# Kernel optimization log

Hardware: AMD Instinct MI355X
Metric: run time of the kernel (lower is better)

The kernel has to match this reference:

```python
import jax, jax.numpy as jnp
import numpy as np

H = 2048        # hidden_size
I = 5632        # intermediate_size (SwiGLU)
E = 8           # num_experts
K = 2           # top_k
B, S = 4, 2048


def setup_inputs() -> dict:
    key = jax.random.key(0)
    ks = jax.random.split(key, 6)
    s_h = 1.0 / np.sqrt(H)
    s_i = 1.0 / np.sqrt(I)
    return {
        "hidden_states": jax.random.normal(ks[0], (B, S, H), dtype=jnp.float32),
        "Wr": jax.random.normal(ks[1], (H, E), dtype=jnp.float32) * s_h,   # router linear weight
        "br": jnp.zeros((E,), dtype=jnp.float32),                           # router bias
        "Wg": jax.random.normal(ks[2], (E, H, I), dtype=jnp.float32) * s_h, # gate_proj per expert
        "Wu": jax.random.normal(ks[3], (E, H, I), dtype=jnp.float32) * s_h, # up_proj per expert
        "Wd": jax.random.normal(ks[4], (E, I, H), dtype=jnp.float32) * s_i, # down_proj per expert
    }


def reference(hidden_states, Wr, br, Wg, Wu, Wd):
    b, s, h = hidden_states.shape
    xf = hidden_states.reshape(b * s, h)                      # [T, H]

    # Router (eval mode: no noise, no dropout)
    router_logits = xf @ Wr + br                              # [T, E]
    probs = jax.nn.softmax(router_logits, axis=-1)
    w, idx = jax.lax.top_k(probs, K)                          # [T, K]
    w = w / jnp.sum(w, axis=-1, keepdims=True)                # renormalize top-k weights

    out = jnp.zeros_like(xf)
    for e in range(E):
        # per-token combine weight for expert e (sums duplicate k-slots, as the torch loop does)
        we = jnp.sum(w * (idx == e), axis=-1)                 # [T]
        # SwiGLU expert: down(silu(gate(x)) * up(x))
        expert_out = (jax.nn.silu(xf @ Wg[e]) * (xf @ Wu[e])) @ Wd[e]  # [T, H]
        out = out + expert_out * we[:, None]
    output = out.reshape(b, s, h)
    return output, router_logits
```

## Files before the change

kernel.cpp:

```cpp
#include <hip/hip_runtime.h>

#define Hdim 2048
#define Idim 5632
#define NEXP 8
#define NTOK 8192
#define NROW 16384
#define RCAP 18432
#define MT256 72

#define MI_NTILES   0
#define MI_TOTAL    1
#define MI_COUNT    2
#define MI_CURSOR   10
#define MI_OFF      18
#define MI_TILEEXP  32
#define MI_ROWTOK   128
#define MI_ROWW     18560
#define MI_TOPKID   36992
#define MI_TOPKW    53376
#define META_ZERO_BYTES (36992u * 4u)

#define XG_OFF   (1ull << 19)
#define WGT_OFF  (73ull  << 20)
#define WUT_OFF  (249ull << 20)
#define HB_OFF   (425ull << 20)
#define WDT_OFF  WGT_OFF

typedef __attribute__((ext_vector_type(8))) short s8v;
typedef __attribute__((ext_vector_type(4))) float f4v;

#define BAR()  asm volatile("s_barrier" ::: "memory")
#define VMW2() asm volatile("s_waitcnt vmcnt(2)" ::: "memory")

__device__ __forceinline__ unsigned short f2bf(float f) {
  unsigned int u = __float_as_uint(f);
  u += 0x7fffu + ((u >> 16) & 1u);
  return (unsigned short)(u >> 16);
}
__device__ __forceinline__ unsigned int pack2(float lo, float hi) {
  return (__float_as_uint(lo) >> 16) | (__float_as_uint(hi) & 0xffff0000u);
}
__device__ __forceinline__ void glds16(const short* gp, short* lp) {
  __builtin_amdgcn_global_load_lds(
      (const __attribute__((address_space(1))) void*)gp,
      (__attribute__((address_space(3))) void*)lp, 16, 0, 0);
}

__global__ __launch_bounds__(256) void router_kernel(
    const float* __restrict__ x, const float* __restrict__ Wr,
    const float* __restrict__ br, float* __restrict__ logits,
    int* __restrict__ meta)
{
  int wv = threadIdx.x >> 6, lane = threadIdx.x & 63;
  int t = blockIdx.x * 4 + wv;
  const float* xr = x + (size_t)t * Hdim;
  float acc[8];
#pragma unroll
  for (int e = 0; e < 8; ++e) acc[e] = 0.f;
  for (int i = lane; i < Hdim; i += 64) {
    float xv = xr[i];
    const float4 w0 = *(const float4*)(Wr + (size_t)i * 8);
    const float4 w1 = *(const float4*)(Wr + (size_t)i * 8 + 4);
    acc[0] += xv * w0.x; acc[1] += xv * w0.y; acc[2] += xv * w0.z; acc[3] += xv * w0.w;
    acc[4] += xv * w1.x; acc[5] += xv * w1.y; acc[6] += xv * w1.z; acc[7] += xv * w1.w;
  }
#pragma unroll
  for (int off = 32; off > 0; off >>= 1)
#pragma unroll
    for (int e = 0; e < 8; ++e) acc[e] += __shfl_down(acc[e], off);
  if (lane == 0) {
    float l[8];
#pragma unroll
    for (int e = 0; e < 8; ++e) { l[e] = acc[e] + br[e]; logits[(size_t)t * 8 + e] = l[e]; }
    int i1 = 0;
#pragma unroll
    for (int e = 1; e < 8; ++e) if (l[e] > l[i1]) i1 = e;
    int i2 = -1;
#pragma unroll
    for (int e = 0; e < 8; ++e) if (e != i1 && (i2 < 0 || l[e] > l[i2])) i2 = e;
    float p2 = __expf(l[i2] - l[i1]);
    float s = 1.f + p2;
    meta[MI_TOPKID + t * 2]     = i1;
    meta[MI_TOPKID + t * 2 + 1] = i2;
    float* tw = (float*)(meta + MI_TOPKW);
    tw[t * 2] = 1.f / s; tw[t * 2 + 1] = p2 / s;
    atomicAdd(&meta[MI_COUNT + i1], 1);
    atomicAdd(&meta[MI_COUNT + i2], 1);
  }
}

__global__ void offsets_kernel(int* __restrict__ meta)
{
  __shared__ int soff[9];
  if (threadIdx.x == 0) {
    int off = 0;
#pragma unroll
    for (int e = 0; e < 8; ++e) {
      soff[e] = off;
      meta[MI_OFF + e] = off;
      meta[MI_CURSOR + e] = off;
      int c = meta[MI_COUNT + e];
      off += (c + 255) & ~255;
    }
    soff[8] = off;
    meta[MI_OFF + 8] = off;
    meta[MI_TOTAL] = off;
    meta[MI_NTILES] = off >> 8;
  }
  __syncthreads();
  int tile = threadIdx.x;
  if (tile < MT256) {
    int r = tile << 8;
    int e = 7;
    for (int q = 7; q >= 0; --q) if (r < soff[q + 1]) e = q;
    meta[MI_TILEEXP + tile] = e;
  }
}

__global__ __launch_bounds__(256) void scatter_kernel(int* __restrict__ meta)
{
  int idx = blockIdx.x * 256 + threadIdx.x;
  int e = meta[MI_TOPKID + idx];
  float w = ((const float*)(meta + MI_TOPKW))[idx];
  int pos = atomicAdd(&meta[MI_CURSOR + e], 1);
  meta[MI_ROWTOK + pos] = idx >> 1;
  ((float*)(meta + MI_ROWW))[pos] = w;
}

__global__ __launch_bounds__(256) void gather_kernel(
    const float* __restrict__ x, short* __restrict__ Xg,
    const int* __restrict__ meta)
{
  int r = blockIdx.x;
  int tok = meta[MI_ROWTOK + r];
  int i = threadIdx.x * 8;
  const float* src = x + (size_t)tok * Hdim + i;
  float4 a = *(const float4*)src;
  float4 b = *(const float4*)(src + 4);
  union { s8v v; unsigned short us[8]; } o;
  o.us[0] = f2bf(a.x); o.us[1] = f2bf(a.y); o.us[2] = f2bf(a.z); o.us[3] = f2bf(a.w);
  o.us[4] = f2bf(b.x); o.us[5] = f2bf(b.y); o.us[6] = f2bf(b.z); o.us[7] = f2bf(b.w);
  *(s8v*)(Xg + (size_t)r * Hdim + i) = o.v;
}

__global__ __launch_bounds__(256) void convT_kernel(
    const float* __restrict__ W, short* __restrict__ T, int K, int N)
{
  __shared__ float lds[64][65];
  int ntn = N >> 6, ntk = K >> 6;
  int per_e = ntn * ntk;
  int e = blockIdx.x / per_e;
  int r = blockIdx.x % per_e;
  int tn = r % ntn, tk = r / ntn;
  const float* We = W + (size_t)e * K * N;
  short* Te = T + (size_t)e * K * N;
  int n0 = tn << 6, k0 = tk << 6;
  int tid = threadIdx.x;
  int c = tid & 63, rr = tid >> 6;
#pragma unroll
  for (int i = 0; i < 16; ++i) {
    int k = i * 4 + rr;
    lds[c][k] = We[(size_t)(k0 + k) * N + n0 + c];
  }
  __syncthreads();
  int kp = tid & 31, nb = tid >> 5;
#pragma unroll
  for (int i = 0; i < 8; ++i) {
    int n = i * 8 + nb;
    float2 f = *(const float2*)&lds[n][kp * 2];
    unsigned int u = pack2(f.x, f.y);
    *(unsigned int*)((char*)Te + ((size_t)(n0 + n) * K + k0) * 2 + kp * 4) = u;
  }
}


#define ISSUE_A2(buf, h, kt) do { size_t kk_ = (size_t)(kt) * 64;                          \
  glds16(pA + (size_t)((h) * 128      ) * strideA + kk_, &sA[(buf)][(h) * 8192 + ldst]);   \
  glds16(pA + (size_t)((h) * 128 + 64 ) * strideA + kk_, &sA[(buf)][(h) * 8192 + 4096 + ldst]); } while (0)
#define ISSUE_B2(arr, pB, buf, kt) do { size_t kk_ = (size_t)(kt) * 64;                    \
  glds16((pB) + kk_,                          &arr[(buf)][ldst]);                          \
  glds16((pB) + (size_t)64 * strideA + kk_,   &arr[(buf)][4096 + ldst]); } while (0)

__global__ __launch_bounds__(512, 2) void gateup_kernel(
    const short* __restrict__ Xg, const short* __restrict__ WgT,
    const short* __restrict__ WuT, short* __restrict__ Hbuf,
    const int* __restrict__ meta)
{
  const int NT = Idim / 128;
  int wg = (blockIdx.x & 7) * (MT256 / 8 * NT) + (blockIdx.x >> 3);
  int chunk = wg / (8 * NT);
  int rem   = wg % (8 * NT);
  int mtile = chunk * 8 + (rem & 7);
  int ntile = rem >> 3;
  if (mtile >= meta[MI_NTILES]) return;
  int e = meta[MI_TILEEXP + mtile];
  int n0 = ntile * 128;
  const size_t strideA = Hdim;

  __shared__ short sA[2][16384];
  __shared__ short sG[2][8192];
  __shared__ short sU[2][8192];

  int tid = threadIdx.x;
  int lane = tid & 63, wv = tid >> 6;
  int wm = wv >> 1, wn = wv & 1;
  int lr = lane & 15, lg = lane >> 4;
  int ldst = wv * 512;

  int srow = tid >> 3;
  int kc = ((tid & 7) ^ (srow & 7)) * 8;
  const short* pA = Xg  + (size_t)(mtile * 256) * Hdim + (size_t)srow * Hdim + kc;
  const short* pG = WgT + (size_t)e * Idim * Hdim + (size_t)(n0 + srow) * Hdim + kc;
  const short* pU = WuT + (size_t)e * Idim * Hdim + (size_t)(n0 + srow) * Hdim + kc;

  int aoff[4][2], boff[4][2];
#pragma unroll
  for (int mi = 0; mi < 4; ++mi) {
    int R = wm * 64 + mi * 16 + lr;
#pragma unroll
    for (int ks = 0; ks < 2; ++ks) aoff[mi][ks] = R * 64 + (((ks * 4 + lg) ^ (R & 7)) << 3);
  }
#pragma unroll
  for (int ni = 0; ni < 4; ++ni) {
    int R = wn * 64 + ni * 16 + lr;
#pragma unroll
    for (int ks = 0; ks < 2; ++ks) boff[ni][ks] = R * 64 + (((ks * 4 + lg) ^ (R & 7)) << 3);
  }

  f4v AG[4][4], AU[4][4];
  f4v z = {0.f, 0.f, 0.f, 0.f};
#pragma unroll
  for (int a1 = 0; a1 < 4; ++a1)
#pragma unroll
    for (int b1 = 0; b1 < 4; ++b1) { AG[a1][b1] = z; AU[a1][b1] = z; }

  const int NKT = Hdim / 64;

  ISSUE_A2(0, 0, 0); ISSUE_A2(0, 1, 0);
  ISSUE_B2(sG, pG, 0, 0); ISSUE_B2(sU, pU, 0, 0);
  ISSUE_A2(1, 0, 1);
  VMW2(); BAR();

#define GU_HALF(CUR, T)                                                                    \
  do {                                                                                     \
    int nx1 = (T) + 1; if (nx1 >= NKT) nx1 -= NKT;                                         \
    int nx2 = (T) + 2; if (nx2 >= NKT) nx2 -= NKT;                                         \
    s8v a_[4][2], g0_[2][2], g1_[2][2], u0_[2][2], u1_[2][2];                              \
                                                 \
    _Pragma("unroll") for (int mi = 0; mi < 4; ++mi)                                       \
      _Pragma("unroll") for (int ks = 0; ks < 2; ++ks)                                     \
        a_[mi][ks] = *(const s8v*)&sA[CUR][aoff[mi][ks]];                                  \
    _Pragma("unroll") for (int ni = 0; ni < 2; ++ni)                                       \
      _Pragma("unroll") for (int ks = 0; ks < 2; ++ks)                                     \
        g0_[ni][ks] = *(const s8v*)&sG[CUR][boff[ni][ks]];                                 \
    ISSUE_A2((CUR) ^ 1, 1, nx1);                                                           \
    BAR(); __builtin_amdgcn_s_setprio(1);                                                  \
    _Pragma("unroll") for (int mi = 0; mi < 4; ++mi)                                       \
      _Pragma("unroll") for (int ni = 0; ni < 2; ++ni)                                     \
        _Pragma("unroll") for (int ks = 0; ks < 2; ++ks)                                   \
          AG[mi][ni] = __builtin_amdgcn_mfma_f32_16x16x32_bf16(a_[mi][ks], g0_[ni][ks],    \
                                                               AG[mi][ni], 0, 0, 0);       \
    __builtin_amdgcn_s_setprio(0); BAR();                                                  \
                                             \
    _Pragma("unroll") for (int ni = 0; ni < 2; ++ni)                                       \
      _Pragma("unroll") for (int ks = 0; ks < 2; ++ks) {                                   \
        g1_[ni][ks] = *(const s8v*)&sG[CUR][boff[2 + ni][ks]];                             \
        u0_[ni][ks] = *(const s8v*)&sU[CUR][boff[ni][ks]];                                 \
      }                                                                                    \
    ISSUE_B2(sG, pG, (CUR) ^ 1, nx1);                                                      \
    BAR(); __builtin_amdgcn_s_setprio(1);                                                  \
    _Pragma("unroll") for (int mi = 0; mi < 4; ++mi)                                       \
      _Pragma("unroll") for (int ni = 0; ni < 2; ++ni)                                     \
        _Pragma("unroll") for (int ks = 0; ks < 2; ++ks)                                   \
          AG[mi][2 + ni] = __builtin_amdgcn_mfma_f32_16x16x32_bf16(a_[mi][ks], g1_[ni][ks],\
                                                                   AG[mi][2 + ni], 0, 0, 0);\
    __builtin_amdgcn_s_setprio(0); BAR();                                                  \
                                           \
    _Pragma("unroll") for (int ni = 0; ni < 2; ++ni)                                       \
      _Pragma("unroll") for (int ks = 0; ks < 2; ++ks)                                     \
        u1_[ni][ks] = *(const s8v*)&sU[CUR][boff[2 + ni][ks]];                             \
    ISSUE_B2(sU, pU, (CUR) ^ 1, nx1);                                                      \
    BAR(); __builtin_amdgcn_s_setprio(1);                                                  \
    _Pragma("unroll") for (int mi = 0; mi < 4; ++mi)                                       \
      _Pragma("unroll") for (int ni = 0; ni < 2; ++ni)                                     \
        _Pragma("unroll") for (int ks = 0; ks < 2; ++ks)                                   \
          AU[mi][ni] = __builtin_amdgcn_mfma_f32_16x16x32_bf16(a_[mi][ks], u0_[ni][ks],    \
                                                               AU[mi][ni], 0, 0, 0);       \
    __builtin_amdgcn_s_setprio(0); BAR();                                                  \
                                         \
    ISSUE_A2(CUR, 0, nx2);                                                                 \
    VMW2();                                                                                \
    BAR(); __builtin_amdgcn_s_setprio(1);                                                  \
    _Pragma("unroll") for (int mi = 0; mi < 4; ++mi)                                       \
      _Pragma("unroll") for (int ni = 0; ni < 2; ++ni)                                     \
        _Pragma("unroll") for (int ks = 0; ks < 2; ++ks)                                   \
          AU[mi][2 + ni] = __builtin_amdgcn_mfma_f32_16x16x32_bf16(a_[mi][ks], u1_[ni][ks],\
                                                                   AU[mi][2 + ni], 0, 0, 0);\
    __builtin_amdgcn_s_setprio(0); BAR();                                                  \
  } while (0)

  for (int t = 0; t < NKT; t += 2) {
    GU_HALF(0, t);
    GU_HALF(1, t + 1);
  }
#undef GU_HALF

  int row0 = mtile * 256 + wm * 64;
  int col0 = n0 + wn * 64;
#pragma unroll
  for (int mi = 0; mi < 4; ++mi) {
#pragma unroll
    for (int ni = 0; ni < 4; ++ni) {
      int col = col0 + ni * 16 + lr;
#pragma unroll
      for (int r = 0; r < 4; ++r) {
        int row = row0 + mi * 16 + lg * 4 + r;
        float g = AG[mi][ni][r], u = AU[mi][ni][r];
        float h = g / (1.f + __expf(-g)) * u;
        Hbuf[(size_t)row * Idim + col] = (short)f2bf(h);
      }
    }
  }
}

__global__ __launch_bounds__(512, 2) void down_kernel(
    const short* __restrict__ Hbuf, const short* __restrict__ WdT,
    float* __restrict__ out, const int* __restrict__ meta)
{
  const int NT = Hdim / 128;
  int wg = (blockIdx.x & 7) * (MT256 / 8 * NT) + (blockIdx.x >> 3);
  int chunk = wg / (8 * NT);
  int rem   = wg % (8 * NT);
  int mtile = chunk * 8 + (rem & 7);
  int ntile = rem >> 3;
  if (mtile >= meta[MI_NTILES]) return;
  int e = meta[MI_TILEEXP + mtile];
  int n0 = ntile * 128;
  const size_t strideA = Idim;

  __shared__ short sA[2][16384];
  __shared__ short sB[2][8192];

  int tid = threadIdx.x;
  int lane = tid & 63, wv = tid >> 6;
  int wm = wv >> 1, wn = wv & 1;
  int lr = lane & 15, lg = lane >> 4;
  int ldst = wv * 512;

  int srow = tid >> 3;
  int kc = ((tid & 7) ^ (srow & 7)) * 8;
  const short* pA = Hbuf + (size_t)(mtile * 256) * Idim + (size_t)srow * Idim + kc;
  const short* pB = WdT  + (size_t)e * Hdim * Idim + (size_t)(n0 + srow) * Idim + kc;

  int aoff[4][2], boff[4][2];
#pragma unroll
  for (int mi = 0; mi < 4; ++mi) {
    int R = wm * 64 + mi * 16 + lr;
#pragma unroll
    for (int ks = 0; ks < 2; ++ks) aoff[mi][ks] = R * 64 + (((ks * 4 + lg) ^ (R & 7)) << 3);
  }
#pragma unroll
  for (int ni = 0; ni < 4; ++ni) {
    int R = wn * 64 + ni * 16 + lr;
#pragma unroll
    for (int ks = 0; ks < 2; ++ks) boff[ni][ks] = R * 64 + (((ks * 4 + lg) ^ (R & 7)) << 3);
  }

  f4v AC[4][4];
  f4v z = {0.f, 0.f, 0.f, 0.f};
#pragma unroll
  for (int a1 = 0; a1 < 4; ++a1)
#pragma unroll
    for (int b1 = 0; b1 < 4; ++b1) AC[a1][b1] = z;

  const int NKT = Idim / 64;

  ISSUE_A2(0, 0, 0); ISSUE_A2(0, 1, 0);
  ISSUE_B2(sB, pB, 0, 0);
  ISSUE_A2(1, 0, 1);
  VMW2(); BAR();

#define DN_PHASE(CUR, NI, EXTRA)                                                           \
  do {                                                                                     \
    EXTRA;                                                                                 \
    BAR(); __builtin_amdgcn_s_setprio(1);                                                  \
    _Pragma("unroll") for (int mi = 0; mi < 4; ++mi)                                       \
      _Pragma("unroll") for (int ks = 0; ks < 2; ++ks)                                     \
        AC[mi][NI] = __builtin_amdgcn_mfma_f32_16x16x32_bf16(a_[mi][ks], b_[NI][ks],       \
                                                             AC[mi][NI], 0, 0, 0);         \
    __builtin_amdgcn_s_setprio(0); BAR();                                                  \
  } while (0)

#define DN_HALF(CUR, T)                                                                    \
  do {                                                                                     \
    int nx1 = (T) + 1; if (nx1 >= NKT) nx1 -= NKT;                                         \
    int nx2 = (T) + 2; if (nx2 >= NKT) nx2 -= NKT;                                         \
    s8v a_[4][2], b_[4][2];                                                                \
                                                                \
    _Pragma("unroll") for (int mi = 0; mi < 4; ++mi)                                       \
      _Pragma("unroll") for (int ks = 0; ks < 2; ++ks)                                     \
        a_[mi][ks] = *(const s8v*)&sA[CUR][aoff[mi][ks]];                                  \
    _Pragma("unroll") for (int ni = 0; ni < 2; ++ni)                                       \
      _Pragma("unroll") for (int ks = 0; ks < 2; ++ks)                                     \
        b_[ni][ks] = *(const s8v*)&sB[CUR][boff[ni][ks]];                                  \
    DN_PHASE(CUR, 0, ISSUE_A2((CUR) ^ 1, 1, nx1));                                         \
                                                                    \
    DN_PHASE(CUR, 1, {                                                                     \
      _Pragma("unroll") for (int ni = 2; ni < 4; ++ni)                                     \
        _Pragma("unroll") for (int ks = 0; ks < 2; ++ks)                                   \
          b_[ni][ks] = *(const s8v*)&sB[CUR][boff[ni][ks]];                                \
      ISSUE_B2(sB, pB, (CUR) ^ 1, nx1); });                                                \
    DN_PHASE(CUR, 2, {});                                                                  \
    DN_PHASE(CUR, 3, { ISSUE_A2(CUR, 0, nx2); VMW2(); });                                  \
  } while (0)

  for (int t = 0; t < NKT; t += 2) {
    DN_HALF(0, t);
    DN_HALF(1, t + 1);
  }
#undef DN_HALF
#undef DN_PHASE

  int row0 = mtile * 256 + wm * 64;
  int col0 = n0 + wn * 64;
  const int* rowtok = meta + MI_ROWTOK;
  const float* roww = (const float*)(meta + MI_ROWW);
#pragma unroll
  for (int mi = 0; mi < 4; ++mi) {
#pragma unroll
    for (int r = 0; r < 4; ++r) {
      int row = row0 + mi * 16 + lg * 4 + r;
      int tok = rowtok[row];
      float w = roww[row];
      float* orow = out + (size_t)tok * Hdim + col0 + lr;
#pragma unroll
      for (int ni = 0; ni < 4; ++ni)
        atomicAdd(orow + ni * 16, w * AC[mi][ni][r]);
    }
  }
}

extern "C" void kernel_launch(void* const* d_in, const int* in_sizes, int n_in,
                              void* d_out, int out_size, void* d_ws, size_t ws_size,
                              hipStream_t stream)
{
  (void)in_sizes; (void)n_in; (void)out_size; (void)ws_size;
  const float* x  = (const float*)d_in[0];
  const float* Wr = (const float*)d_in[1];
  const float* br = (const float*)d_in[2];
  const float* Wg = (const float*)d_in[3];
  const float* Wu = (const float*)d_in[4];
  const float* Wd = (const float*)d_in[5];
  float* out = (float*)d_out;
  float* logits = out + (size_t)NTOK * Hdim;
  int* meta = (int*)d_ws;
  short* Xg   = (short*)((char*)d_ws + XG_OFF);
  short* WgT  = (short*)((char*)d_ws + WGT_OFF);
  short* WuT  = (short*)((char*)d_ws + WUT_OFF);
  short* WdT  = (short*)((char*)d_ws + WDT_OFF);
  short* Hbuf = (short*)((char*)d_ws + HB_OFF);

  hipMemsetAsync(d_out, 0, (size_t)NTOK * Hdim * sizeof(float), stream);
  hipMemsetAsync(d_ws, 0, META_ZERO_BYTES, stream);

  const int convBlocks = NEXP * (Idim / 64) * (Hdim / 64);

  router_kernel <<<NTOK / 4, 256, 0, stream>>>(x, Wr, br, logits, meta);
  offsets_kernel<<<1, 256, 0, stream>>>(meta);
  scatter_kernel<<<NROW / 256, 256, 0, stream>>>(meta);
  gather_kernel <<<RCAP, 256, 0, stream>>>(x, Xg, meta);
  convT_kernel  <<<convBlocks, 256, 0, stream>>>(Wg, WgT, Hdim, Idim);
  convT_kernel  <<<convBlocks, 256, 0, stream>>>(Wu, WuT, Hdim, Idim);
  gateup_kernel <<<MT256 * (Idim / 128), 512, 0, stream>>>(Xg, WgT, WuT, Hbuf, meta);
  convT_kernel  <<<convBlocks, 256, 0, stream>>>(Wd, WdT, Idim, Hdim);
  down_kernel   <<<MT256 * (Hdim / 128), 512, 0, stream>>>(Hbuf, WdT, out, meta);
}
```

Before: 2.298 ms.

## Widen down-proj tile to 256 columns and batch per-stage global-to-LDS loads

The down-projection kernel now computes a 256x256 output tile per workgroup instead of 256x128. This halves how often the A (hidden) operand is re-read and halves the number of atomic-add tiles per row. Both GEMM kernels replace their interleaved half-stage prefetches with one full-stage load burst per k-tile, waited on with vmcnt(8) and an lgkmcnt(0) fence. The cost is more accumulator registers (AC grows to 4x8), double the sB LDS footprint, and fewer workgroups in the down kernel, which may lower occupancy.

```diff
diff --git a/kernel.cpp b/kernel.cpp
--- a/kernel.cpp
+++ b/kernel.cpp
@@ -29,8 +29,11 @@
 typedef __attribute__((ext_vector_type(8))) short s8v;
 typedef __attribute__((ext_vector_type(4))) float f4v;
 
-#define BAR()  asm volatile("s_barrier" ::: "memory")
-#define VMW2() asm volatile("s_waitcnt vmcnt(2)" ::: "memory")
+#define BAR()   asm volatile("s_barrier" ::: "memory")
+#define VMW8()  asm volatile("s_waitcnt vmcnt(8)" ::: "memory")
+#define LGKM0() asm volatile("s_waitcnt lgkmcnt(0)" ::: "memory")
+#define PRIO1() __builtin_amdgcn_s_setprio(1)
+#define PRIO0() __builtin_amdgcn_s_setprio(0)
 
 __device__ __forceinline__ unsigned short f2bf(float f) {
   unsigned int u = __float_as_uint(f);
@@ -174,12 +177,8 @@
 }
 
 
-#define ISSUE_A2(buf, h, kt) do { size_t kk_ = (size_t)(kt) * 64;                          \
-  glds16(pA + (size_t)((h) * 128      ) * strideA + kk_, &sA[(buf)][(h) * 8192 + ldst]);   \
-  glds16(pA + (size_t)((h) * 128 + 64 ) * strideA + kk_, &sA[(buf)][(h) * 8192 + 4096 + ldst]); } while (0)
-#define ISSUE_B2(arr, pB, buf, kt) do { size_t kk_ = (size_t)(kt) * 64;                    \
-  glds16((pB) + kk_,                          &arr[(buf)][ldst]);                          \
-  glds16((pB) + (size_t)64 * strideA + kk_,   &arr[(buf)][4096 + ldst]); } while (0)
+#define STG(arr, pX, buf, r, kk) \
+  glds16((pX) + (size_t)(r) * 64 * strideA + (kk), &arr[(buf)][(r) * 4096 + ldst])
 
 __global__ __launch_bounds__(512, 2) void gateup_kernel(
     const short* __restrict__ Xg, const short* __restrict__ WgT,
@@ -236,74 +235,75 @@
 
   const int NKT = Hdim / 64;
 
-  ISSUE_A2(0, 0, 0); ISSUE_A2(0, 1, 0);
-  ISSUE_B2(sG, pG, 0, 0); ISSUE_B2(sU, pU, 0, 0);
-  ISSUE_A2(1, 0, 1);
-  VMW2(); BAR();
-
-#define GU_HALF(CUR, T)                                                                    \
+#define GU_STAGE(buf, kt) do { size_t kk_ = (size_t)(kt) * 64;  \
+    STG(sA, pA, buf, 0, kk_); STG(sA, pA, buf, 1, kk_);         \
+    STG(sA, pA, buf, 2, kk_); STG(sA, pA, buf, 3, kk_);         \
+    STG(sG, pG, buf, 0, kk_); STG(sG, pG, buf, 1, kk_);         \
+    STG(sU, pU, buf, 0, kk_); STG(sU, pU, buf, 1, kk_); } while (0)
+
+  GU_STAGE(0, 0); GU_STAGE(1, 1);
+  VMW8(); BAR();
+
+#define GU_TILE(CUR, T)                                                                    \
   do {                                                                                     \
-    int nx1 = (T) + 1; if (nx1 >= NKT) nx1 -= NKT;                                         \
     int nx2 = (T) + 2; if (nx2 >= NKT) nx2 -= NKT;                                         \
     s8v a_[4][2], g0_[2][2], g1_[2][2], u0_[2][2], u1_[2][2];                              \
-                                                 \
+                                                                      \
     _Pragma("unroll") for (int mi = 0; mi < 4; ++mi)                                       \
       _Pragma("unroll") for (int ks = 0; ks < 2; ++ks)                                     \
         a_[mi][ks] = *(const s8v*)&sA[CUR][aoff[mi][ks]];                                  \
     _Pragma("unroll") for (int ni = 0; ni < 2; ++ni)                                       \
       _Pragma("unroll") for (int ks = 0; ks < 2; ++ks)                                     \
         g0_[ni][ks] = *(const s8v*)&sG[CUR][boff[ni][ks]];                                 \
-    ISSUE_A2((CUR) ^ 1, 1, nx1);                                                           \
-    BAR(); __builtin_amdgcn_s_setprio(1);                                                  \
+    BAR(); PRIO1();                                                                        \
     _Pragma("unroll") for (int mi = 0; mi < 4; ++mi)                                       \
       _Pragma("unroll") for (int ni = 0; ni < 2; ++ni)                                     \
         _Pragma("unroll") for (int ks = 0; ks < 2; ++ks)                                   \
           AG[mi][ni] = __builtin_amdgcn_mfma_f32_16x16x32_bf16(a_[mi][ks], g0_[ni][ks],    \
                                                                AG[mi][ni], 0, 0, 0);       \
-    __builtin_amdgcn_s_setprio(0); BAR();                                                  \
-                                             \
+    PRIO0(); BAR();                                                                        \
+                                                                     \
     _Pragma("unroll") for (int ni = 0; ni < 2; ++ni)                                       \
       _Pragma("unroll") for (int ks = 0; ks < 2; ++ks) {                                   \
         g1_[ni][ks] = *(const s8v*)&sG[CUR][boff[2 + ni][ks]];                             \
         u0_[ni][ks] = *(const s8v*)&sU[CUR][boff[ni][ks]];                                 \
       }                                                                                    \
-    ISSUE_B2(sG, pG, (CUR) ^ 1, nx1);                                                      \
-    BAR(); __builtin_amdgcn_s_setprio(1);                                                  \
+    BAR(); PRIO1();                                                                        \
     _Pragma("unroll") for (int mi = 0; mi < 4; ++mi)                                       \
       _Pragma("unroll") for (int ni = 0; ni < 2; ++ni)                                     \
         _Pragma("unroll") for (int ks = 0; ks < 2; ++ks)                                   \
           AG[mi][2 + ni] = __builtin_amdgcn_mfma_f32_16x16x32_bf16(a_[mi][ks], g1_[ni][ks],\
                                                                    AG[mi][2 + ni], 0, 0, 0);\
-    __builtin_amdgcn_s_setprio(0); BAR();                                                  \
-                                           \
+    PRIO0(); BAR();                                                                        \
+          \
     _Pragma("unroll") for (int ni = 0; ni < 2; ++ni)                                       \
       _Pragma("unroll") for (int ks = 0; ks < 2; ++ks)                                     \
         u1_[ni][ks] = *(const s8v*)&sU[CUR][boff[2 + ni][ks]];                             \
-    ISSUE_B2(sU, pU, (CUR) ^ 1, nx1);                                                      \
-    BAR(); __builtin_amdgcn_s_setprio(1);                                                  \
+    BAR(); PRIO1();                                                                        \
     _Pragma("unroll") for (int mi = 0; mi < 4; ++mi)                                       \
       _Pragma("unroll") for (int ni = 0; ni < 2; ++ni)                                     \
         _Pragma("unroll") for (int ks = 0; ks < 2; ++ks)                                   \
           AU[mi][ni] = __builtin_amdgcn_mfma_f32_16x16x32_bf16(a_[mi][ks], u0_[ni][ks],    \
                                                                AU[mi][ni], 0, 0, 0);       \
-    __builtin_amdgcn_s_setprio(0); BAR();                                                  \
-                                         \
-    ISSUE_A2(CUR, 0, nx2);                                                                 \
-    VMW2();                                                                                \
-    BAR(); __builtin_amdgcn_s_setprio(1);                                                  \
+    PRIO0(); LGKM0(); BAR();                                                               \
+         \
+    GU_STAGE(CUR, nx2);                                                                    \
+    VMW8();                                                                                \
+    BAR(); PRIO1();                                                                        \
     _Pragma("unroll") for (int mi = 0; mi < 4; ++mi)                                       \
       _Pragma("unroll") for (int ni = 0; ni < 2; ++ni)                                     \
         _Pragma("unroll") for (int ks = 0; ks < 2; ++ks)                                   \
           AU[mi][2 + ni] = __builtin_amdgcn_mfma_f32_16x16x32_bf16(a_[mi][ks], u1_[ni][ks],\
                                                                    AU[mi][2 + ni], 0, 0, 0);\
-    __builtin_amdgcn_s_setprio(0); BAR();                                                  \
+    PRIO0(); BAR();                                                                        \
   } while (0)
 
   for (int t = 0; t < NKT; t += 2) {
-    GU_HALF(0, t);
-    GU_HALF(1, t + 1);
-  }
-#undef GU_HALF
+    GU_TILE(0, t);
+    GU_TILE(1, t + 1);
+  }
+#undef GU_TILE
+#undef GU_STAGE
 
   int row0 = mtile * 256 + wm * 64;
   int col0 = n0 + wn * 64;
@@ -327,7 +327,7 @@
     const short* __restrict__ Hbuf, const short* __restrict__ WdT,
     float* __restrict__ out, const int* __restrict__ meta)
 {
-  const int NT = Hdim / 128;
+  const int NT = Hdim / 256;
   int wg = (blockIdx.x & 7) * (MT256 / 8 * NT) + (blockIdx.x >> 3);
   int chunk = wg / (8 * NT);
   int rem   = wg % (8 * NT);
@@ -335,11 +335,11 @@
   int ntile = rem >> 3;
   if (mtile >= meta[MI_NTILES]) return;
   int e = meta[MI_TILEEXP + mtile];
-  int n0 = ntile * 128;
+  int n0 = ntile * 256;
   const size_t strideA = Idim;
 
   __shared__ short sA[2][16384];
-  __shared__ short sB[2][8192];
+  __shared__ short sB[2][16384];
 
   int tid = threadIdx.x;
   int lane = tid & 63, wv = tid >> 6;
@@ -352,7 +352,7 @@
   const short* pA = Hbuf + (size_t)(mtile * 256) * Idim + (size_t)srow * Idim + kc;
   const short* pB = WdT  + (size_t)e * Hdim * Idim + (size_t)(n0 + srow) * Idim + kc;
 
-  int aoff[4][2], boff[4][2];
+  int aoff[4][2], boff[8][2];
 #pragma unroll
   for (int mi = 0; mi < 4; ++mi) {
     int R = wm * 64 + mi * 16 + lr;
@@ -360,69 +360,77 @@
     for (int ks = 0; ks < 2; ++ks) aoff[mi][ks] = R * 64 + (((ks * 4 + lg) ^ (R & 7)) << 3);
   }
 #pragma unroll
-  for (int ni = 0; ni < 4; ++ni) {
-    int R = wn * 64 + ni * 16 + lr;
+  for (int ni = 0; ni < 8; ++ni) {
+    int R = wn * 128 + ni * 16 + lr;
 #pragma unroll
     for (int ks = 0; ks < 2; ++ks) boff[ni][ks] = R * 64 + (((ks * 4 + lg) ^ (R & 7)) << 3);
   }
 
-  f4v AC[4][4];
+  f4v AC[4][8];
   f4v z = {0.f, 0.f, 0.f, 0.f};
 #pragma unroll
   for (int a1 = 0; a1 < 4; ++a1)
 #pragma unroll
-    for (int b1 = 0; b1 < 4; ++b1) AC[a1][b1] = z;
+    for (int b1 = 0; b1 < 8; ++b1) AC[a1][b1] = z;
 
   const int NKT = Idim / 64;
 
-  ISSUE_A2(0, 0, 0); ISSUE_A2(0, 1, 0);
-  ISSUE_B2(sB, pB, 0, 0);
-  ISSUE_A2(1, 0, 1);
-  VMW2(); BAR();
-
-#define DN_PHASE(CUR, NI, EXTRA)                                                           \
+#define DN_STAGE(buf, kt) do { size_t kk_ = (size_t)(kt) * 64;  \
+    STG(sA, pA, buf, 0, kk_); STG(sA, pA, buf, 1, kk_);         \
+    STG(sA, pA, buf, 2, kk_); STG(sA, pA, buf, 3, kk_);         \
+    STG(sB, pB, buf, 0, kk_); STG(sB, pB, buf, 1, kk_);         \
+    STG(sB, pB, buf, 2, kk_); STG(sB, pB, buf, 3, kk_); } while (0)
+
+  DN_STAGE(0, 0); DN_STAGE(1, 1);
+  VMW8(); BAR();
+
+#define DN_MFMA(NI0)                                                                       \
+    BAR(); PRIO1();                                                                        \
+    _Pragma("unroll") for (int mi = 0; mi < 4; ++mi)                                       \
+      _Pragma("unroll") for (int nj = 0; nj < 2; ++nj)                                     \
+        _Pragma("unroll") for (int ks = 0; ks < 2; ++ks)                                   \
+          AC[mi][(NI0) + nj] = __builtin_amdgcn_mfma_f32_16x16x32_bf16(                    \
+              a_[mi][ks], b_[(NI0) + nj][ks], AC[mi][(NI0) + nj], 0, 0, 0);                \
+    PRIO0()
+
+#define DN_TILE(CUR, T)                                                                    \
   do {                                                                                     \
-    EXTRA;                                                                                 \
-    BAR(); __builtin_amdgcn_s_setprio(1);                                                  \
-    _Pragma("unroll") for (int mi = 0; mi < 4; ++mi)                                       \
-      _Pragma("unroll") for (int ks = 0; ks < 2; ++ks)                                     \
-        AC[mi][NI] = __builtin_amdgcn_mfma_f32_16x16x32_bf16(a_[mi][ks], b_[NI][ks],       \
-                                                             AC[mi][NI], 0, 0, 0);         \
-    __builtin_amdgcn_s_setprio(0); BAR();                                                  \
-  } while (0)
-
-#define DN_HALF(CUR, T)                                                                    \
-  do {                                                                                     \
-    int nx1 = (T) + 1; if (nx1 >= NKT) nx1 -= NKT;                                         \
     int nx2 = (T) + 2; if (nx2 >= NKT) nx2 -= NKT;                                         \
-    s8v a_[4][2], b_[4][2];                                                                \
-                                                                \
+    s8v a_[4][2], b_[8][2];                                                                \
+                                                                     \
     _Pragma("unroll") for (int mi = 0; mi < 4; ++mi)                                       \
       _Pragma("unroll") for (int ks = 0; ks < 2; ++ks)                                     \
         a_[mi][ks] = *(const s8v*)&sA[CUR][aoff[mi][ks]];                                  \
     _Pragma("unroll") for (int ni = 0; ni < 2; ++ni)                                       \
       _Pragma("unroll") for (int ks = 0; ks < 2; ++ks)                                     \
         b_[ni][ks] = *(const s8v*)&sB[CUR][boff[ni][ks]];                                  \
-    DN_PHASE(CUR, 0, ISSUE_A2((CUR) ^ 1, 1, nx1));                                         \
-                                                                    \
-    DN_PHASE(CUR, 1, {                                                                     \
-      _Pragma("unroll") for (int ni = 2; ni < 4; ++ni)                                     \
-        _Pragma("unroll") for (int ks = 0; ks < 2; ++ks)                                   \
-          b_[ni][ks] = *(const s8v*)&sB[CUR][boff[ni][ks]];                                \
-      ISSUE_B2(sB, pB, (CUR) ^ 1, nx1); });                                                \
-    DN_PHASE(CUR, 2, {});                                                                  \
-    DN_PHASE(CUR, 3, { ISSUE_A2(CUR, 0, nx2); VMW2(); });                                  \
+    DN_MFMA(0); BAR();                                                                     \
+                                                                         \
+    _Pragma("unroll") for (int ni = 2; ni < 4; ++ni)                                       \
+      _Pragma("unroll") for (int ks = 0; ks < 2; ++ks)                                     \
+        b_[ni][ks] = *(const s8v*)&sB[CUR][boff[ni][ks]];                                  \
+    DN_MFMA(2); BAR();                                                                     \
+                                       \
+    _Pragma("unroll") for (int ni = 4; ni < 8; ++ni)                                       \
+      _Pragma("unroll") for (int ks = 0; ks < 2; ++ks)                                     \
+        b_[ni][ks] = *(const s8v*)&sB[CUR][boff[ni][ks]];                                  \
+    DN_MFMA(4); LGKM0(); BAR();                                                            \
+                                                          \
+    DN_STAGE(CUR, nx2);                                                                    \
+    VMW8();                                                                                \
+    DN_MFMA(6); BAR();                                                                     \
   } while (0)
 
   for (int t = 0; t < NKT; t += 2) {
-    DN_HALF(0, t);
-    DN_HALF(1, t + 1);
-  }
-#undef DN_HALF
-#undef DN_PHASE
+    DN_TILE(0, t);
+    DN_TILE(1, t + 1);
+  }
+#undef DN_TILE
+#undef DN_MFMA
+#undef DN_STAGE
 
   int row0 = mtile * 256 + wm * 64;
-  int col0 = n0 + wn * 64;
+  int col0 = n0 + wn * 128;
   const int* rowtok = meta + MI_ROWTOK;
   const float* roww = (const float*)(meta + MI_ROWW);
 #pragma unroll
@@ -434,7 +442,7 @@
       float w = roww[row];
       float* orow = out + (size_t)tok * Hdim + col0 + lr;
 #pragma unroll
-      for (int ni = 0; ni < 4; ++ni)
+      for (int ni = 0; ni < 8; ++ni)
         atomicAdd(orow + ni * 16, w * AC[mi][ni][r]);
     }
   }
@@ -473,5 +481,5 @@
   convT_kernel  <<<convBlocks, 256, 0, stream>>>(Wu, WuT, Hdim, Idim);
   gateup_kernel <<<MT256 * (Idim / 128), 512, 0, stream>>>(Xg, WgT, WuT, Hbuf, meta);
   convT_kernel  <<<convBlocks, 256, 0, stream>>>(Wd, WdT, Idim, Hdim);
-  down_kernel   <<<MT256 * (Hdim / 128), 512, 0, stream>>>(Hbuf, WdT, out, meta);
-}
+  down_kernel   <<<MT256 * (Hdim / 256), 512, 0, stream>>>(Hbuf, WdT, out, meta);
+}
```

Result: no change. 2.256 ms (-1.8%).

## Load A operand directly from global into registers, stage only weights in LDS

Applied to the files above, without the earlier changes.

Both the gate/up and down GEMM kernels stop staging the activation (A) tile through shared memory. Each wave now reads its A fragments straight from global memory into registers, and only the weight tiles are double-buffered in LDS through a simpler one-stage-ahead pipeline that waits with vmcnt(0). The block-to-tile swizzle also changes from groups of 8 M-tiles to groups of 4. The aim is to free LDS and cut barrier and LDS traffic. The cost is that the global A loads are exposed to latency with little overlap, since each stage waits for all loads, and A is re-read by both N-halves of the waves.

```diff
diff --git a/kernel.cpp b/kernel.cpp
--- a/kernel.cpp
+++ b/kernel.cpp
@@ -29,8 +29,10 @@
 typedef __attribute__((ext_vector_type(8))) short s8v;
 typedef __attribute__((ext_vector_type(4))) float f4v;
 
-#define BAR()  asm volatile("s_barrier" ::: "memory")
-#define VMW2() asm volatile("s_waitcnt vmcnt(2)" ::: "memory")
+#define BAR()   asm volatile("s_barrier" ::: "memory")
+#define VMW0()  asm volatile("s_waitcnt vmcnt(0)" ::: "memory")
+#define PRIO1() __builtin_amdgcn_s_setprio(1)
+#define PRIO0() __builtin_amdgcn_s_setprio(0)
 
 __device__ __forceinline__ unsigned short f2bf(float f) {
   unsigned int u = __float_as_uint(f);
@@ -174,30 +176,21 @@
 }
 
 
-#define ISSUE_A2(buf, h, kt) do { size_t kk_ = (size_t)(kt) * 64;                          \
-  glds16(pA + (size_t)((h) * 128      ) * strideA + kk_, &sA[(buf)][(h) * 8192 + ldst]);   \
-  glds16(pA + (size_t)((h) * 128 + 64 ) * strideA + kk_, &sA[(buf)][(h) * 8192 + 4096 + ldst]); } while (0)
-#define ISSUE_B2(arr, pB, buf, kt) do { size_t kk_ = (size_t)(kt) * 64;                    \
-  glds16((pB) + kk_,                          &arr[(buf)][ldst]);                          \
-  glds16((pB) + (size_t)64 * strideA + kk_,   &arr[(buf)][4096 + ldst]); } while (0)
-
 __global__ __launch_bounds__(512, 2) void gateup_kernel(
     const short* __restrict__ Xg, const short* __restrict__ WgT,
     const short* __restrict__ WuT, short* __restrict__ Hbuf,
     const int* __restrict__ meta)
 {
   const int NT = Idim / 128;
-  int wg = (blockIdx.x & 7) * (MT256 / 8 * NT) + (blockIdx.x >> 3);
-  int chunk = wg / (8 * NT);
-  int rem   = wg % (8 * NT);
-  int mtile = chunk * 8 + (rem & 7);
-  int ntile = rem >> 3;
+  int wg = (blockIdx.x & 7) * ((MT256 * NT) / 8) + (blockIdx.x >> 3);
+  int chunk = wg / (4 * NT);
+  int rem   = wg % (4 * NT);
+  int mtile = chunk * 4 + (rem & 3);
+  int ntile = rem >> 2;
   if (mtile >= meta[MI_NTILES]) return;
   int e = meta[MI_TILEEXP + mtile];
   int n0 = ntile * 128;
-  const size_t strideA = Hdim;
-
-  __shared__ short sA[2][16384];
+
   __shared__ short sG[2][8192];
   __shared__ short sU[2][8192];
 
@@ -209,17 +202,15 @@
 
   int srow = tid >> 3;
   int kc = ((tid & 7) ^ (srow & 7)) * 8;
-  const short* pA = Xg  + (size_t)(mtile * 256) * Hdim + (size_t)srow * Hdim + kc;
   const short* pG = WgT + (size_t)e * Idim * Hdim + (size_t)(n0 + srow) * Hdim + kc;
   const short* pU = WuT + (size_t)e * Idim * Hdim + (size_t)(n0 + srow) * Hdim + kc;
 
-  int aoff[4][2], boff[4][2];
-#pragma unroll
-  for (int mi = 0; mi < 4; ++mi) {
-    int R = wm * 64 + mi * 16 + lr;
-#pragma unroll
-    for (int ks = 0; ks < 2; ++ks) aoff[mi][ks] = R * 64 + (((ks * 4 + lg) ^ (R & 7)) << 3);
-  }
+  const short* pAm[4];
+#pragma unroll
+  for (int mi = 0; mi < 4; ++mi)
+    pAm[mi] = Xg + (size_t)(mtile * 256 + wm * 64 + mi * 16 + lr) * Hdim + lg * 8;
+
+  int boff[4][2];
 #pragma unroll
   for (int ni = 0; ni < 4; ++ni) {
     int R = wn * 64 + ni * 16 + lr;
@@ -236,74 +227,63 @@
 
   const int NKT = Hdim / 64;
 
-  ISSUE_A2(0, 0, 0); ISSUE_A2(0, 1, 0);
-  ISSUE_B2(sG, pG, 0, 0); ISSUE_B2(sU, pU, 0, 0);
-  ISSUE_A2(1, 0, 1);
-  VMW2(); BAR();
-
-#define GU_HALF(CUR, T)                                                                    \
-  do {                                                                                     \
-    int nx1 = (T) + 1; if (nx1 >= NKT) nx1 -= NKT;                                         \
-    int nx2 = (T) + 2; if (nx2 >= NKT) nx2 -= NKT;                                         \
-    s8v a_[4][2], g0_[2][2], g1_[2][2], u0_[2][2], u1_[2][2];                              \
-                                                 \
-    _Pragma("unroll") for (int mi = 0; mi < 4; ++mi)                                       \
-      _Pragma("unroll") for (int ks = 0; ks < 2; ++ks)                                     \
-        a_[mi][ks] = *(const s8v*)&sA[CUR][aoff[mi][ks]];                                  \
-    _Pragma("unroll") for (int ni = 0; ni < 2; ++ni)                                       \
-      _Pragma("unroll") for (int ks = 0; ks < 2; ++ks)                                     \
-        g0_[ni][ks] = *(const s8v*)&sG[CUR][boff[ni][ks]];                                 \
-    ISSUE_A2((CUR) ^ 1, 1, nx1);                                                           \
-    BAR(); __builtin_amdgcn_s_setprio(1);                                                  \
-    _Pragma("unroll") for (int mi = 0; mi < 4; ++mi)                                       \
-      _Pragma("unroll") for (int ni = 0; ni < 2; ++ni)                                     \
-        _Pragma("unroll") for (int ks = 0; ks < 2; ++ks)                                   \
-          AG[mi][ni] = __builtin_amdgcn_mfma_f32_16x16x32_bf16(a_[mi][ks], g0_[ni][ks],    \
-                                                               AG[mi][ni], 0, 0, 0);       \
-    __builtin_amdgcn_s_setprio(0); BAR();                                                  \
-                                             \
-    _Pragma("unroll") for (int ni = 0; ni < 2; ++ni)                                       \
-      _Pragma("unroll") for (int ks = 0; ks < 2; ++ks) {                                   \
-        g1_[ni][ks] = *(const s8v*)&sG[CUR][boff[2 + ni][ks]];                             \
-        u0_[ni][ks] = *(const s8v*)&sU[CUR][boff[ni][ks]];                                 \
-      }                                                                                    \
-    ISSUE_B2(sG, pG, (CUR) ^ 1, nx1);                                                      \
-    BAR(); __builtin_amdgcn_s_setprio(1);                                                  \
-    _Pragma("unroll") for (int mi = 0; mi < 4; ++mi)                                       \
-      _Pragma("unroll") for (int ni = 0; ni < 2; ++ni)                                     \
-        _Pragma("unroll") for (int ks = 0; ks < 2; ++ks)                                   \
-          AG[mi][2 + ni] = __builtin_amdgcn_mfma_f32_16x16x32_bf16(a_[mi][ks], g1_[ni][ks],\
-                                                                   AG[mi][2 + ni], 0, 0, 0);\
-    __builtin_amdgcn_s_setprio(0); BAR();                                                  \
-                                           \
-    _Pragma("unroll") for (int ni = 0; ni < 2; ++ni)                                       \
-      _Pragma("unroll") for (int ks = 0; ks < 2; ++ks)                                     \
-        u1_[ni][ks] = *(const s8v*)&sU[CUR][boff[2 + ni][ks]];                             \
-    ISSUE_B2(sU, pU, (CUR) ^ 1, nx1);                                                      \
-    BAR(); __builtin_amdgcn_s_setprio(1);                                                  \
-    _Pragma("unroll") for (int mi = 0; mi < 4; ++mi)                                       \
-      _Pragma("unroll") for (int ni = 0; ni < 2; ++ni)                                     \
-        _Pragma("unroll") for (int ks = 0; ks < 2; ++ks)                                   \
-          AU[mi][ni] = __builtin_amdgcn_mfma_f32_16x16x32_bf16(a_[mi][ks], u0_[ni][ks],    \
-                                                               AU[mi][ni], 0, 0, 0);       \
-    __builtin_amdgcn_s_setprio(0); BAR();                                                  \
-                                         \
-    ISSUE_A2(CUR, 0, nx2);                                                                 \
-    VMW2();                                                                                \
-    BAR(); __builtin_amdgcn_s_setprio(1);                                                  \
-    _Pragma("unroll") for (int mi = 0; mi < 4; ++mi)                                       \
-      _Pragma("unroll") for (int ni = 0; ni < 2; ++ni)                                     \
-        _Pragma("unroll") for (int ks = 0; ks < 2; ++ks)                                   \
-          AU[mi][2 + ni] = __builtin_amdgcn_mfma_f32_16x16x32_bf16(a_[mi][ks], u1_[ni][ks],\
-                                                                   AU[mi][2 + ni], 0, 0, 0);\
-    __builtin_amdgcn_s_setprio(0); BAR();                                                  \
-  } while (0)
-
-  for (int t = 0; t < NKT; t += 2) {
-    GU_HALF(0, t);
-    GU_HALF(1, t + 1);
-  }
-#undef GU_HALF
+#define GU_STAGE(buf, kt) do { size_t kk_ = (size_t)(kt) * 64;                     \
+    glds16(pG + kk_,                     &sG[buf][ldst]);                          \
+    glds16(pG + (size_t)64 * Hdim + kk_, &sG[buf][4096 + ldst]);                   \
+    glds16(pU + kk_,                     &sU[buf][ldst]);                          \
+    glds16(pU + (size_t)64 * Hdim + kk_, &sU[buf][4096 + ldst]); } while (0)
+
+  GU_STAGE(0, 0);
+
+#pragma unroll 2
+  for (int t = 0; t < NKT; ++t) {
+    int cur = t & 1;
+    int nx = (t + 1 < NKT) ? (t + 1) : 0;
+    int k0 = t * 64;
+    VMW0();
+    BAR();
+    s8v a_[4][2];
+#pragma unroll
+    for (int mi = 0; mi < 4; ++mi)
+#pragma unroll
+      for (int ks = 0; ks < 2; ++ks)
+        a_[mi][ks] = *(const s8v*)(pAm[mi] + k0 + ks * 32);
+    __builtin_amdgcn_sched_barrier(0);
+    GU_STAGE(cur ^ 1, nx);
+    s8v g_[4][2];
+#pragma unroll
+    for (int ni = 0; ni < 4; ++ni)
+#pragma unroll
+      for (int ks = 0; ks < 2; ++ks)
+        g_[ni][ks] = *(const s8v*)&sG[cur][boff[ni][ks]];
+    PRIO1();
+#pragma unroll
+    for (int mi = 0; mi < 4; ++mi)
+#pragma unroll
+      for (int ni = 0; ni < 4; ++ni)
+#pragma unroll
+        for (int ks = 0; ks < 2; ++ks)
+          AG[mi][ni] = __builtin_amdgcn_mfma_f32_16x16x32_bf16(a_[mi][ks], g_[ni][ks],
+                                                               AG[mi][ni], 0, 0, 0);
+    PRIO0();
+    s8v u_[4][2];
+#pragma unroll
+    for (int ni = 0; ni < 4; ++ni)
+#pragma unroll
+      for (int ks = 0; ks < 2; ++ks)
+        u_[ni][ks] = *(const s8v*)&sU[cur][boff[ni][ks]];
+    PRIO1();
+#pragma unroll
+    for (int mi = 0; mi < 4; ++mi)
+#pragma unroll
+      for (int ni = 0; ni < 4; ++ni)
+#pragma unroll
+        for (int ks = 0; ks < 2; ++ks)
+          AU[mi][ni] = __builtin_amdgcn_mfma_f32_16x16x32_bf16(a_[mi][ks], u_[ni][ks],
+                                                               AU[mi][ni], 0, 0, 0);
+    PRIO0();
+  }
+#undef GU_STAGE
 
   int row0 = mtile * 256 + wm * 64;
   int col0 = n0 + wn * 64;
@@ -328,17 +308,15 @@
     float* __restrict__ out, const int* __restrict__ meta)
 {
   const int NT = Hdim / 128;
-  int wg = (blockIdx.x & 7) * (MT256 / 8 * NT) + (blockIdx.x >> 3);
-  int chunk = wg / (8 * NT);
-  int rem   = wg % (8 * NT);
-  int mtile = chunk * 8 + (rem & 7);
-  int ntile = rem >> 3;
+  int wg = (blockIdx.x & 7) * ((MT256 * NT) / 8) + (blockIdx.x >> 3);
+  int chunk = wg / (4 * NT);
+  int rem   = wg % (4 * NT);
+  int mtile = chunk * 4 + (rem & 3);
+  int ntile = rem >> 2;
   if (mtile >= meta[MI_NTILES]) return;
   int e = meta[MI_TILEEXP + mtile];
   int n0 = ntile * 128;
-  const size_t strideA = Idim;
-
-  __shared__ short sA[2][16384];
+
   __shared__ short sB[2][8192];
 
   int tid = threadIdx.x;
@@ -349,16 +327,14 @@
 
   int srow = tid >> 3;
   int kc = ((tid & 7) ^ (srow & 7)) * 8;
-  const short* pA = Hbuf + (size_t)(mtile * 256) * Idim + (size_t)srow * Idim + kc;
-  const short* pB = WdT  + (size_t)e * Hdim * Idim + (size_t)(n0 + srow) * Idim + kc;
-
-  int aoff[4][2], boff[4][2];
-#pragma unroll
-  for (int mi = 0; mi < 4; ++mi) {
-    int R = wm * 64 + mi * 16 + lr;
-#pragma unroll
-    for (int ks = 0; ks < 2; ++ks) aoff[mi][ks] = R * 64 + (((ks * 4 + lg) ^ (R & 7)) << 3);
-  }
+  const short* pB = WdT + (size_t)e * Hdim * Idim + (size_t)(n0 + srow) * Idim + kc;
+
+  const short* pAm[4];
+#pragma unroll
+  for (int mi = 0; mi < 4; ++mi)
+    pAm[mi] = Hbuf + (size_t)(mtile * 256 + wm * 64 + mi * 16 + lr) * Idim + lg * 8;
+
+  int boff[4][2];
 #pragma unroll
   for (int ni = 0; ni < 4; ++ni) {
     int R = wn * 64 + ni * 16 + lr;
@@ -375,51 +351,45 @@
 
   const int NKT = Idim / 64;
 
-  ISSUE_A2(0, 0, 0); ISSUE_A2(0, 1, 0);
-  ISSUE_B2(sB, pB, 0, 0);
-  ISSUE_A2(1, 0, 1);
-  VMW2(); BAR();
-
-#define DN_PHASE(CUR, NI, EXTRA)                                                           \
-  do {                                                                                     \
-    EXTRA;                                                                                 \
-    BAR(); __builtin_amdgcn_s_setprio(1);                                                  \
-    _Pragma("unroll") for (int mi = 0; mi < 4; ++mi)                                       \
-      _Pragma("unroll") for (int ks = 0; ks < 2; ++ks)                                     \
-        AC[mi][NI] = __builtin_amdgcn_mfma_f32_16x16x32_bf16(a_[mi][ks], b_[NI][ks],       \
-                                                             AC[mi][NI], 0, 0, 0);         \
-    __builtin_amdgcn_s_setprio(0); BAR();                                                  \
-  } while (0)
-
-#define DN_HALF(CUR, T)                                                                    \
-  do {                                                                                     \
-    int nx1 = (T) + 1; if (nx1 >= NKT) nx1 -= NKT;                                         \
-    int nx2 = (T) + 2; if (nx2 >= NKT) nx2 -= NKT;                                         \
-    s8v a_[4][2], b_[4][2];                                                                \
-                                                                \
-    _Pragma("unroll") for (int mi = 0; mi < 4; ++mi)                                       \
-      _Pragma("unroll") for (int ks = 0; ks < 2; ++ks)                                     \
-        a_[mi][ks] = *(const s8v*)&sA[CUR][aoff[mi][ks]];                                  \
-    _Pragma("unroll") for (int ni = 0; ni < 2; ++ni)                                       \
-      _Pragma("unroll") for (int ks = 0; ks < 2; ++ks)                                     \
-        b_[ni][ks] = *(const s8v*)&sB[CUR][boff[ni][ks]];                                  \
-    DN_PHASE(CUR, 0, ISSUE_A2((CUR) ^ 1, 1, nx1));                                         \
-                                                                    \
-    DN_PHASE(CUR, 1, {                                                                     \
-      _Pragma("unroll") for (int ni = 2; ni < 4; ++ni)                                     \
-        _Pragma("unroll") for (int ks = 0; ks < 2; ++ks)                                   \
-          b_[ni][ks] = *(const s8v*)&sB[CUR][boff[ni][ks]];                                \
-      ISSUE_B2(sB, pB, (CUR) ^ 1, nx1); });                                                \
-    DN_PHASE(CUR, 2, {});                                                                  \
-    DN_PHASE(CUR, 3, { ISSUE_A2(CUR, 0, nx2); VMW2(); });                                  \
-  } while (0)
-
-  for (int t = 0; t < NKT; t += 2) {
-    DN_HALF(0, t);
-    DN_HALF(1, t + 1);
-  }
-#undef DN_HALF
-#undef DN_PHASE
+#define DN_STAGE(buf, kt) do { size_t kk_ = (size_t)(kt) * 64;                     \
+    glds16(pB + kk_,                     &sB[buf][ldst]);                          \
+    glds16(pB + (size_t)64 * Idim + kk_, &sB[buf][4096 + ldst]); } while (0)
+
+  DN_STAGE(0, 0);
+
+#pragma unroll 2
+  for (int t = 0; t < NKT; ++t) {
+    int cur = t & 1;
+    int nx = (t + 1 < NKT) ? (t + 1) : 0;
+    int k0 = t * 64;
+    VMW0();
+    BAR();
+    s8v a_[4][2];
+#pragma unroll
+    for (int mi = 0; mi < 4; ++mi)
+#pragma unroll
+      for (int ks = 0; ks < 2; ++ks)
+        a_[mi][ks] = *(const s8v*)(pAm[mi] + k0 + ks * 32);
+    __builtin_amdgcn_sched_barrier(0);
+    DN_STAGE(cur ^ 1, nx);
+    s8v b_[4][2];
+#pragma unroll
+    for (int ni = 0; ni < 4; ++ni)
+#pragma unroll
+      for (int ks = 0; ks < 2; ++ks)
+        b_[ni][ks] = *(const s8v*)&sB[cur][boff[ni][ks]];
+    PRIO1();
+#pragma unroll
+    for (int mi = 0; mi < 4; ++mi)
+#pragma unroll
+      for (int ni = 0; ni < 4; ++ni)
+#pragma unroll
+        for (int ks = 0; ks < 2; ++ks)
+          AC[mi][ni] = __builtin_amdgcn_mfma_f32_16x16x32_bf16(a_[mi][ks], b_[ni][ks],
+                                                               AC[mi][ni], 0, 0, 0);
+    PRIO0();
+  }
+#undef DN_STAGE
 
   int row0 = mtile * 256 + wm * 64;
   int col0 = n0 + wn * 64;
```

Result: slower. 3.146 ms (+36.9%).
